# Kernel tuning notes

Hardware: AMD Instinct MI355X
Metric: run time of the kernel (lower is better)

## Reference

```python
import jax, jax.numpy as jnp
import numpy as np

N_EMBD = 768
N_HEAD = 12
EPS = 1e-5


def _layernorm(x, g, b):
    mu = jnp.mean(x, axis=-1, keepdims=True)
    var = jnp.var(x, axis=-1, keepdims=True)
    return (x - mu) * jax.lax.rsqrt(var + EPS) * g + b


def setup_inputs() -> dict:
    key = jax.random.key(0)
    ks = jax.random.split(key, 12)
    C = N_EMBD
    s = 0.02
    return {
        "x": jax.random.normal(ks[0], (1, 4096, C), dtype=jnp.float32),
        "ln1_g": jnp.ones((C,), jnp.float32),
        "ln1_b": jnp.zeros((C,), jnp.float32),
        "w_attn": jax.random.normal(ks[1], (C, 3 * C), jnp.float32) * s,
        "b_attn": jnp.zeros((3 * C,), jnp.float32),
        "w_ao": jax.random.normal(ks[2], (C, C), jnp.float32) * s,
        "b_ao": jnp.zeros((C,), jnp.float32),
        "ln2_g": jnp.ones((C,), jnp.float32),
        "ln2_b": jnp.zeros((C,), jnp.float32),
        "w_fc": jax.random.normal(ks[3], (C, 4 * C), jnp.float32) * s,
        "b_fc": jnp.zeros((4 * C,), jnp.float32),
        "w_proj": jax.random.normal(ks[4], (4 * C, C), jnp.float32) * s,
        "b_proj": jnp.zeros((C,), jnp.float32),
    }


def reference(x, ln1_g, ln1_b, w_attn, b_attn, w_ao, b_ao,
              ln2_g, ln2_b, w_fc, b_fc, w_proj, b_proj):
    B, T, C = x.shape
    H = N_HEAD
    D = C // H

    # ---- attention sub-block ----
    h = _layernorm(x, ln1_g, ln1_b)
    qkv = h @ w_attn + b_attn                      # [B,T,3C]
    q, k, v = jnp.split(qkv, 3, axis=-1)
    q = q.reshape(B, T, H, D).transpose(0, 2, 1, 3)  # [B,H,T,D]
    k = k.reshape(B, T, H, D).transpose(0, 2, 1, 3)
    v = v.reshape(B, T, H, D).transpose(0, 2, 1, 3)
    att = jnp.einsum('bhqd,bhkd->bhqk', q, k) * (1.0 / jnp.sqrt(jnp.float32(D)))
    att = jax.nn.softmax(att, axis=-1)             # no causal mask in source
    y = jnp.einsum('bhqk,bhkd->bhqd', att, v)      # [B,H,T,D]
    y = y.transpose(0, 2, 1, 3).reshape(B, T, C)
    x = x + y @ w_ao + b_ao

    # ---- MLP sub-block ----
    h = _layernorm(x, ln2_g, ln2_b)
    h = jax.nn.gelu(h @ w_fc + b_fc, approximate=False)  # torch F.gelu = exact
    x = x + h @ w_proj + b_proj
    return x
```

## Files before the change

### kernel.cpp

```cpp
#include <hip/hip_runtime.h>
#include <hip/hip_bf16.h>
#include <cstdint>
#include <cstddef>

typedef __hip_bfloat16 bf16;
typedef __attribute__((ext_vector_type(8))) short short8;
typedef __attribute__((ext_vector_type(4))) float f32x4;
typedef __attribute__((ext_vector_type(16))) float f32x16;

#define C_EMBD 768
#define C3     2304
#define T_SEQ  4096
#define NHEAD  12
#define KVSPLIT 2

__device__ __forceinline__ void load16(const void* g, void* lds) {
  __builtin_amdgcn_global_load_lds(
      (const __attribute__((address_space(1))) uint32_t*)g,
      (__attribute__((address_space(3))) uint32_t*)lds, 16, 0, 0);
}

__device__ __forceinline__ short f2bf_bits(float x) {
  union { bf16 h; short s; } u; u.h = __float2bfloat16(x); return u.s;
}

__device__ __forceinline__ float bfbits2f(short s) {
  union { uint32_t u; float f; } u; u.u = ((uint32_t)(unsigned short)s) << 16; return u.f;
}

__device__ __forceinline__ float max3f(float a, float b, float c) {
  float d;
  asm("v_max3_f32 %0, %1, %2, %3" : "=v"(d) : "v"(a), "v"(b), "v"(c));
  return d;
}

#if __has_builtin(__builtin_amdgcn_exp2f)
#define QK_SCALE (0.125f * 1.44269504088896340736f)
__device__ __forceinline__ float expx(float x) { return __builtin_amdgcn_exp2f(x); }
#else
#define QK_SCALE 0.125f
__device__ __forceinline__ float expx(float x) { return __expf(x); }
#endif

__global__ __launch_bounds__(256) void ln_kernel(const float* __restrict__ x,
    const float* __restrict__ g, const float* __restrict__ b, bf16* __restrict__ out) {
  const int row = blockIdx.x;
  const int tid = threadIdx.x;
  const int lane = tid & 63, wave = tid >> 6;
  const float* xr = x + (size_t)row * C_EMBD;
  float v[3];
  #pragma unroll
  for (int i = 0; i < 3; ++i) v[i] = xr[tid + i * 256];
  float s = v[0] + v[1] + v[2];
  #pragma unroll
  for (int o = 1; o < 64; o <<= 1) s += __shfl_xor(s, o, 64);
  __shared__ float red[4];
  if (lane == 0) red[wave] = s;
  __syncthreads();
  const float mu = (red[0] + red[1] + red[2] + red[3]) * (1.0f / C_EMBD);
  float d0 = v[0] - mu, d1 = v[1] - mu, d2 = v[2] - mu;
  float q = d0 * d0 + d1 * d1 + d2 * d2;
  #pragma unroll
  for (int o = 1; o < 64; o <<= 1) q += __shfl_xor(q, o, 64);
  __syncthreads();
  if (lane == 0) red[wave] = q;
  __syncthreads();
  const float var = (red[0] + red[1] + red[2] + red[3]) * (1.0f / C_EMBD);
  const float rs = rsqrtf(var + 1e-5f);
  #pragma unroll
  for (int i = 0; i < 3; ++i) {
    int c = tid + i * 256;
    out[(size_t)row * C_EMBD + c] = __float2bfloat16((v[i] - mu) * rs * g[c] + b[c]);
  }
}

__global__ __launch_bounds__(256) void transpose4_kernel(
    const float* __restrict__ wA, bf16* __restrict__ oA,
    const float* __restrict__ wB, bf16* __restrict__ oB,
    const float* __restrict__ wC, bf16* __restrict__ oC,
    const float* __restrict__ wD, bf16* __restrict__ oD) {
  __shared__ float tile[32][33];
  int b = blockIdx.x;
  const float* in; bf16* out; int R, C;
  if (b < 1728)      { in = wA; out = oA; R = 768;  C = 2304; }
  else if (b < 2304) { b -= 1728; in = wB; out = oB; R = 768;  C = 768;  }
  else if (b < 4608) { b -= 2304; in = wC; out = oC; R = 768;  C = 3072; }
  else               { b -= 4608; in = wD; out = oD; R = 3072; C = 768;  }
  const int ntx = C / 32;
  const int bx = (b % ntx) * 32;
  const int by = (b / ntx) * 32;
  const int tx = threadIdx.x, ty = threadIdx.y;
  #pragma unroll
  for (int i = 0; i < 32; i += 8)
    tile[ty + i][tx] = in[(size_t)(by + ty + i) * C + bx + tx];
  __syncthreads();
  #pragma unroll
  for (int i = 0; i < 32; i += 8)
    out[(size_t)(bx + ty + i) * R + by + tx] = __float2bfloat16(tile[tx][ty + i]);
}

template <int EPI>
__global__ __launch_bounds__(256, 2) void gemm_bt(
    const bf16* __restrict__ A, const bf16* __restrict__ BT,
    const float* __restrict__ bias, const float* __restrict__ res,
    void* __restrict__ outp, float* __restrict__ outp2, int M, int N, int Ks, int Kst) {
  __shared__ __align__(16) short sA[128 * 32];
  __shared__ __align__(16) short sB[128 * 32];
  const int tid = threadIdx.x;
  const int wave = tid >> 6, lane = tid & 63;
  const int qr = lane >> 4, qm = lane & 15;
  const int wr = wave >> 1, wc = wave & 1;
  const int tM = blockIdx.y * 128, tN = blockIdx.x * 128;
  const int z = (EPI == 4) ? blockIdx.z : 0;

  f32x4 acc[4][4] = {};

  const int srow = tid >> 2;
  const int scol = (tid & 3) * 8;
  const bf16* gA = A + (size_t)z * Ks + (size_t)(tM + srow) * Kst + scol;
  const bf16* gB = BT + (size_t)z * Ks + (size_t)(tN + srow) * Kst + scol;
  char* ldsAw = (char*)sA + wave * 1024;
  char* ldsBw = (char*)sB + wave * 1024;
  const size_t rowskip = (size_t)64 * Kst;

  const int nk = Ks >> 5;
  for (int k0 = 0; k0 < nk; ++k0) {
    __syncthreads();
    load16(gA, ldsAw);
    load16(gA + rowskip, ldsAw + 4096);
    load16(gB, ldsBw);
    load16(gB + rowskip, ldsBw + 4096);
    gA += 32; gB += 32;
    __syncthreads();
    short8 a[4], bb[4];
    #pragma unroll
    for (int i = 0; i < 4; ++i) {
      a[i]  = *(const short8*)&sA[(wr * 64 + i * 16 + qm) * 32 + qr * 8];
      bb[i] = *(const short8*)&sB[(wc * 64 + i * 16 + qm) * 32 + qr * 8];
    }
    #pragma unroll
    for (int mi = 0; mi < 4; ++mi)
      #pragma unroll
      for (int ni = 0; ni < 4; ++ni)
        acc[mi][ni] = __builtin_amdgcn_mfma_f32_16x16x32_bf16(a[mi], bb[ni], acc[mi][ni], 0, 0, 0);
  }

  float* outf = (float*)outp;
  bf16* outh = (bf16*)outp;
  float* po = (EPI == 4) ? ((z == 0) ? (float*)outp : outp2) : nullptr;
  #pragma unroll
  for (int mi = 0; mi < 4; ++mi) {
    #pragma unroll
    for (int ni = 0; ni < 4; ++ni) {
      const int col = tN + wc * 64 + ni * 16 + qm;
      const float bv = (EPI == 4) ? 0.f : bias[col];
      #pragma unroll
      for (int r = 0; r < 4; ++r) {
        const int row = tM + wr * 64 + mi * 16 + qr * 4 + r;
        const size_t idx = (size_t)row * N + col;
        float v = acc[mi][ni][r] + bv;
        if constexpr (EPI == 4) {
          po[idx] = v;
        } else if constexpr (EPI == 1) {
          outf[idx] = v + res[idx];
        } else if constexpr (EPI == 2) {
          v = 0.5f * v * (1.0f + erff(v * 0.70710678118654752f));
          outh[idx] = __float2bfloat16(v);
        } else {
          outh[idx] = __float2bfloat16(v);
        }
      }
    }
  }
}

__global__ __launch_bounds__(256) void splitk_combine(const float* p0,
    const float* __restrict__ p1, const float* __restrict__ res,
    const float* __restrict__ bias, float* out) {
  const int row = blockIdx.x;
  const int tid = threadIdx.x;
  #pragma unroll
  for (int i = 0; i < 3; ++i) {
    const int c = tid + i * 256;
    const size_t idx = (size_t)row * C_EMBD + c;
    out[idx] = p0[idx] + p1[idx] + res[idx] + bias[c];
  }
}

__global__ __launch_bounds__(256, 2) void attn_kernel(const bf16* __restrict__ qkv,
                                                      float* __restrict__ pacc,
                                                      float* __restrict__ pml) {
  __shared__ __align__(16) char sKb[2 * 8192];
  __shared__ __align__(16) char sVb[2 * 8192];
  __shared__ float sRed[4 * 32];

  const int tid = threadIdx.x;
  const int wave = tid >> 6, lane = tid & 63;
  const int qi = lane & 31;
  const int hi = lane >> 5;
  const int hi16 = hi * 16;
  const int head = blockIdx.y;
  const int z = blockIdx.z;
  const int qw = blockIdx.x * 128 + wave * 32;

  short8 qf[4];
  {
    const bf16* qrow = qkv + (size_t)(qw + qi) * C3 + head * 64;
    #pragma unroll
    for (int kd = 0; kd < 4; ++kd) {
      short8 v = *(const short8*)(qrow + kd * 16 + hi * 8);
      #pragma unroll
      for (int i = 0; i < 8; ++i) v[i] = f2bf_bits(bfbits2f(v[i]) * QK_SCALE);
      qf[kd] = v;
    }
  }

  f32x16 acc0 = {}, acc1 = {};
  float m = -3.0e38f, l = 0.f;
  short8 pfrag[4];

  const int nt = (T_SEQ / 64) / KVSPLIT;
  const size_t tilestep = (size_t)64 * C3;
  const size_t zoff = (size_t)z * nt * tilestep;
  const int ksrow = tid >> 3;
  const int kswz = ((tid & 7) ^ (ksrow & 7)) * 8;
  const bf16* gk_base = qkv + zoff + (size_t)ksrow * C3 + C_EMBD + head * 64 + kswz;
  const int vp = tid & 31;
  const int vd0 = (tid >> 5) * 8;
  const bf16* gv_base = qkv + zoff + (size_t)(2 * vp) * C3 + 2 * C_EMBD + head * 64 + vd0;

  const int krow0 = qi * 128;
  const int krow_swz = (qi & 7) << 4;
  const int d1 = 32 + qi;
  const int vs0 = ((qi & 7) ^ ((qi >> 3) & 7)) << 4;
  const int vs1 = ((d1 & 7) ^ ((d1 >> 3) & 7)) << 4;

  short8 v0 = *(const short8*)gv_base;
  short8 v1 = *(const short8*)(gv_base + C3);
  load16(gk_base, sKb + wave * 1024);
  load16(gk_base + (size_t)32 * C3, sKb + wave * 1024 + 4096);

  for (int t = 0; t < nt; ++t) {
    const int cur = t & 1;
    char* bK = sKb + cur * 8192;
    char* bV = sVb + cur * 8192;

    __syncthreads();

    #pragma unroll
    for (int j = 0; j < 8; ++j) {
      const int d = vd0 + j;
      const int vs = ((d & 7) ^ ((d >> 3) & 7)) << 4;
      const uint32_t packed = (uint32_t)(unsigned short)v0[j] |
                              ((uint32_t)(unsigned short)v1[j] << 16);
      *(uint32_t*)(bV + d * 128 + ((vp * 4) ^ vs)) = packed;
    }

    if (t + 1 < nt) {
      const bf16* gv = gv_base + (size_t)(t + 1) * tilestep;
      v0 = *(const short8*)gv;
      v1 = *(const short8*)(gv + C3);
      const bf16* gk = gk_base + (size_t)(t + 1) * tilestep;
      char* bKn = sKb + (cur ^ 1) * 8192;
      load16(gk, bKn + wave * 1024);
      load16(gk + (size_t)32 * C3, bKn + wave * 1024 + 4096);
    }

    f32x16 s0 = {}, s1 = {};
    __builtin_amdgcn_s_setprio(1);
    #pragma unroll
    for (int kd = 0; kd < 4; ++kd) {
      const int off = (kd * 32 + hi16) ^ krow_swz;
      short8 ka0 = *(const short8*)(bK + krow0 + off);
      short8 ka1 = *(const short8*)(bK + 4096 + krow0 + off);
      s0 = __builtin_amdgcn_mfma_f32_32x32x16_bf16(ka0, qf[kd], s0, 0, 0, 0);
      s1 = __builtin_amdgcn_mfma_f32_32x32x16_bf16(ka1, qf[kd], s1, 0, 0, 0);
    }

    if (t > 0) {
      char* bVp = sVb + (cur ^ 1) * 8192;
      #pragma unroll
      for (int kk = 0; kk < 4; ++kk) {
        const int voff = (kk * 32 + hi16);
        short8 vb0 = *(const short8*)(bVp + qi * 128 + (voff ^ vs0));
        short8 vb1 = *(const short8*)(bVp + d1 * 128 + (voff ^ vs1));
        acc0 = __builtin_amdgcn_mfma_f32_32x32x16_bf16(pfrag[kk], vb0, acc0, 0, 0, 0);
        acc1 = __builtin_amdgcn_mfma_f32_32x32x16_bf16(pfrag[kk], vb1, acc1, 0, 0, 0);
      }
    }
    __builtin_amdgcn_s_setprio(0);

    float t8[8];
    #pragma unroll
    for (int i = 0; i < 8; ++i) t8[i] = max3f(s0[i], s0[i + 8], s1[i]);
    float t4[4];
    #pragma unroll
    for (int i = 0; i < 4; ++i) t4[i] = max3f(t8[2 * i], t8[2 * i + 1], s1[8 + i]);
    float t2[2];
    #pragma unroll
    for (int i = 0; i < 2; ++i) t2[i] = max3f(t4[2 * i], t4[2 * i + 1], s1[12 + i]);
    const float t1 = max3f(t2[0], t2[1], s1[14]);
    const float tmx = fmaxf(t1, s1[15]);
    float pmax;
    {
      float a0 = tmx, a1 = tmx;
      asm("v_permlane32_swap_b32 %0, %1" : "+v"(a0), "+v"(a1));
      pmax = fmaxf(a0, a1);
    }

    if (__any(pmax - m > 8.0f)) {
      const float mn = fmaxf(m, pmax);
      const float sc = expx(m - mn);
      l *= sc;
      if (lane < 32) sRed[wave * 32 + qi] = sc;
      #pragma unroll
      for (int r = 0; r < 16; ++r) {
        const float sv = sRed[wave * 32 + ((r & 3) + 8 * (r >> 2) + hi * 4)];
        acc0[r] *= sv; acc1[r] *= sv;
      }
      m = mn;
    }

    float red[16];
    #pragma unroll
    for (int r = 0; r < 16; ++r) { s0[r] = expx(s0[r] - m); s1[r] = expx(s1[r] - m); }
    #pragma unroll
    for (int r = 0; r < 16; ++r) red[r] = s0[r] + s1[r];
    #pragma unroll
    for (int w = 8; w >= 1; w >>= 1)
      #pragma unroll
      for (int r = 0; r < w; ++r) red[r] += red[r + w];
    {
      float a0 = red[0], a1 = red[0];
      asm("v_permlane32_swap_b32 %0, %1" : "+v"(a0), "+v"(a1));
      l += a0 + a1;
    }

    #pragma unroll
    for (int b = 0; b < 2; ++b) {
      const f32x16 sb = b ? s1 : s0;
      uint32_t pk[8];
      #pragma unroll
      for (int g = 0; g < 4; ++g) {
        asm("v_cvt_pk_bf16_f32 %0, %1, %2" : "=v"(pk[2 * g])     : "v"(sb[4 * g + 0]), "v"(sb[4 * g + 1]));
        asm("v_cvt_pk_bf16_f32 %0, %1, %2" : "=v"(pk[2 * g + 1]) : "v"(sb[4 * g + 2]), "v"(sb[4 * g + 3]));
      }
      #pragma unroll
      for (int kbl = 0; kbl < 2; ++kbl) {
        uint32_t w0 = pk[4 * kbl + 0], w2 = pk[4 * kbl + 2];
        asm("v_permlane32_swap_b32 %0, %1" : "+v"(w0), "+v"(w2));
        uint32_t w1 = pk[4 * kbl + 1], w3 = pk[4 * kbl + 3];
        asm("v_permlane32_swap_b32 %0, %1" : "+v"(w1), "+v"(w3));
        union { uint32_t u[4]; short8 v; } pu;
        pu.u[0] = w0; pu.u[1] = w1; pu.u[2] = w2; pu.u[3] = w3;
        pfrag[b * 2 + kbl] = pu.v;
      }
    }
  }

  __syncthreads();
  {
    char* bVl = sVb + ((nt - 1) & 1) * 8192;
    __builtin_amdgcn_s_setprio(1);
    #pragma unroll
    for (int kk = 0; kk < 4; ++kk) {
      const int voff = (kk * 32 + hi16);
      short8 vb0 = *(const short8*)(bVl + qi * 128 + (voff ^ vs0));
      short8 vb1 = *(const short8*)(bVl + d1 * 128 + (voff ^ vs1));
      acc0 = __builtin_amdgcn_mfma_f32_32x32x16_bf16(pfrag[kk], vb0, acc0, 0, 0, 0);
      acc1 = __builtin_amdgcn_mfma_f32_32x32x16_bf16(pfrag[kk], vb1, acc1, 0, 0, 0);
    }
    __builtin_amdgcn_s_setprio(0);
  }

  float* pa = pacc + ((size_t)z * T_SEQ + qw) * C_EMBD + head * 64;
  #pragma unroll
  for (int r = 0; r < 16; ++r) {
    const int q = (r & 3) + 8 * (r >> 2) + hi * 4;
    pa[(size_t)q * C_EMBD + qi]      = acc0[r];
    pa[(size_t)q * C_EMBD + 32 + qi] = acc1[r];
  }
  if (lane < 32) {
    float2* mlp = (float2*)pml;
    mlp[((size_t)z * NHEAD + head) * T_SEQ + qw + qi] = make_float2(m, l);
  }
}

__global__ __launch_bounds__(256) void attn_combine(const float* __restrict__ pacc,
    const float* __restrict__ pml, bf16* __restrict__ out) {
  const int q = blockIdx.x;
  const int tid = threadIdx.x;
  const float2* mlp = (const float2*)pml;
  #pragma unroll
  for (int i = 0; i < 3; ++i) {
    const int c = tid + i * 256;
    const int h = c >> 6;
    const float2 ml0 = mlp[(size_t)h * T_SEQ + q];
    const float2 ml1 = mlp[((size_t)NHEAD + h) * T_SEQ + q];
    const float M = fmaxf(ml0.x, ml1.x);
    const float w0 = expx(ml0.x - M), w1 = expx(ml1.x - M);
    const float inv = 1.0f / (ml0.y * w0 + ml1.y * w1);
    const float a0 = pacc[(size_t)q * C_EMBD + c];
    const float a1 = pacc[(size_t)T_SEQ * C_EMBD + (size_t)q * C_EMBD + c];
    out[(size_t)q * C_EMBD + c] = __float2bfloat16((a0 * w0 + a1 * w1) * inv);
  }
}

extern "C" void kernel_launch(void* const* d_in, const int* in_sizes, int n_in,
                              void* d_out, int out_size, void* d_ws, size_t ws_size,
                              hipStream_t stream) {
  const float* x      = (const float*)d_in[0];
  const float* ln1_g  = (const float*)d_in[1];
  const float* ln1_b  = (const float*)d_in[2];
  const float* w_attn = (const float*)d_in[3];
  const float* b_attn = (const float*)d_in[4];
  const float* w_ao   = (const float*)d_in[5];
  const float* b_ao   = (const float*)d_in[6];
  const float* ln2_g  = (const float*)d_in[7];
  const float* ln2_b  = (const float*)d_in[8];
  const float* w_fc   = (const float*)d_in[9];
  const float* b_fc   = (const float*)d_in[10];
  const float* w_proj = (const float*)d_in[11];
  const float* b_proj = (const float*)d_in[12];

  char* ws = (char*)d_ws;
  size_t off = 0;
  auto alloc = [&](size_t nbytes) {
    char* p = ws + off;
    off += (nbytes + 255) & ~(size_t)255;
    return p;
  };
  bf16* wT_attn = (bf16*)alloc((size_t)C3 * C_EMBD * 2);
  bf16* wT_ao   = (bf16*)alloc((size_t)C_EMBD * C_EMBD * 2);
  bf16* wT_fc   = (bf16*)alloc((size_t)4 * C_EMBD * C_EMBD * 2);
  bf16* wT_proj = (bf16*)alloc((size_t)C_EMBD * 4 * C_EMBD * 2);
  bf16* h       = (bf16*)alloc((size_t)T_SEQ * C_EMBD * 2);
  bf16* qkv     = (bf16*)alloc((size_t)T_SEQ * C3 * 2);
  bf16* y       = (bf16*)alloc((size_t)T_SEQ * C_EMBD * 2);
  float* x1     = (float*)alloc((size_t)T_SEQ * C_EMBD * 4);
  bf16* hf      = (bf16*)alloc((size_t)T_SEQ * 4 * C_EMBD * 2);
  float* pml    = (float*)alloc((size_t)KVSPLIT * NHEAD * T_SEQ * 2 * 4);
  float* pacc   = (float*)hf;
  float* pp0    = (float*)d_out;
  float* pp1    = (float*)qkv;
  (void)ws_size; (void)in_sizes; (void)n_in; (void)out_size;

  transpose4_kernel<<<6912, dim3(32, 8), 0, stream>>>(w_attn, wT_attn, w_ao, wT_ao,
                                                      w_fc, wT_fc, w_proj, wT_proj);

  ln_kernel<<<T_SEQ, 256, 0, stream>>>(x, ln1_g, ln1_b, h);
  gemm_bt<0><<<dim3(C3 / 128, T_SEQ / 128), 256, 0, stream>>>(h, wT_attn, b_attn, nullptr, qkv,
                                                              nullptr, T_SEQ, C3, C_EMBD, C_EMBD);
  attn_kernel<<<dim3(T_SEQ / 128, NHEAD, KVSPLIT), 256, 0, stream>>>(qkv, pacc, pml);
  attn_combine<<<T_SEQ, 256, 0, stream>>>(pacc, pml, y);
  gemm_bt<1><<<dim3(C_EMBD / 128, T_SEQ / 128), 256, 0, stream>>>(y, wT_ao, b_ao, x, x1,
                                                                  nullptr, T_SEQ, C_EMBD,
                                                                  C_EMBD, C_EMBD);
  ln_kernel<<<T_SEQ, 256, 0, stream>>>(x1, ln2_g, ln2_b, h);
  gemm_bt<2><<<dim3(4 * C_EMBD / 128, T_SEQ / 128), 256, 0, stream>>>(h, wT_fc, b_fc, nullptr, hf,
                                                                      nullptr, T_SEQ, 4 * C_EMBD,
                                                                      C_EMBD, C_EMBD);
  gemm_bt<4><<<dim3(C_EMBD / 128, T_SEQ / 128, 2), 256, 0, stream>>>(hf, wT_proj, nullptr, nullptr,
                                                                     pp0, pp1, T_SEQ, C_EMBD,
                                                                     2 * C_EMBD, 4 * C_EMBD);
  splitk_combine<<<T_SEQ, 256, 0, stream>>>(pp0, pp1, x1, b_proj, (float*)d_out);
}
```

Before: 235.9 us.

## Double-buffer GEMM LDS tiles and split-K attention output projection fused into LN2

Converts the GEMM main loop to a two-stage LDS double buffer, so the next K-slice's global-to-LDS loads are issued while the current slice's MFMAs run, with one barrier per iteration instead of two. The attention output projection now runs as a split-K GEMM over two halves, giving a grid of twice as many blocks for this small-N GEMM. A new fused kernel sums the two partials, residual and bias, writes x1, and applies the second layernorm, which replaces the separate LN launch. Costs are doubled LDS per block, which could reduce occupancy, plus extra partial-buffer traffic through the reused hf workspace.

```diff
diff --git a/kernel.cpp b/kernel.cpp
--- a/kernel.cpp
+++ b/kernel.cpp
@@ -51,6 +51,45 @@
   float v[3];
   #pragma unroll
   for (int i = 0; i < 3; ++i) v[i] = xr[tid + i * 256];
+  float s = v[0] + v[1] + v[2];
+  #pragma unroll
+  for (int o = 1; o < 64; o <<= 1) s += __shfl_xor(s, o, 64);
+  __shared__ float red[4];
+  if (lane == 0) red[wave] = s;
+  __syncthreads();
+  const float mu = (red[0] + red[1] + red[2] + red[3]) * (1.0f / C_EMBD);
+  float d0 = v[0] - mu, d1 = v[1] - mu, d2 = v[2] - mu;
+  float q = d0 * d0 + d1 * d1 + d2 * d2;
+  #pragma unroll
+  for (int o = 1; o < 64; o <<= 1) q += __shfl_xor(q, o, 64);
+  __syncthreads();
+  if (lane == 0) red[wave] = q;
+  __syncthreads();
+  const float var = (red[0] + red[1] + red[2] + red[3]) * (1.0f / C_EMBD);
+  const float rs = rsqrtf(var + 1e-5f);
+  #pragma unroll
+  for (int i = 0; i < 3; ++i) {
+    int c = tid + i * 256;
+    out[(size_t)row * C_EMBD + c] = __float2bfloat16((v[i] - mu) * rs * g[c] + b[c]);
+  }
+}
+
+__global__ __launch_bounds__(256) void ln2_fused_kernel(
+    const float* __restrict__ pa0, const float* __restrict__ pa1,
+    const float* __restrict__ x, const float* __restrict__ b_ao,
+    const float* __restrict__ g, const float* __restrict__ b,
+    bf16* __restrict__ out, float* __restrict__ x1) {
+  const int row = blockIdx.x;
+  const int tid = threadIdx.x;
+  const int lane = tid & 63, wave = tid >> 6;
+  float v[3];
+  #pragma unroll
+  for (int i = 0; i < 3; ++i) {
+    const int c = tid + i * 256;
+    const size_t idx = (size_t)row * C_EMBD + c;
+    v[i] = pa0[idx] + pa1[idx] + x[idx] + b_ao[c];
+    x1[idx] = v[i];
+  }
   float s = v[0] + v[1] + v[2];
   #pragma unroll
   for (int o = 1; o < 64; o <<= 1) s += __shfl_xor(s, o, 64);
@@ -104,8 +143,8 @@
     const bf16* __restrict__ A, const bf16* __restrict__ BT,
     const float* __restrict__ bias, const float* __restrict__ res,
     void* __restrict__ outp, float* __restrict__ outp2, int M, int N, int Ks, int Kst) {
-  __shared__ __align__(16) short sA[128 * 32];
-  __shared__ __align__(16) short sB[128 * 32];
+  __shared__ __align__(16) short sA[2][128 * 32];
+  __shared__ __align__(16) short sB[2][128 * 32];
   const int tid = threadIdx.x;
   const int wave = tid >> 6, lane = tid & 63;
   const int qr = lane >> 4, qm = lane & 15;
@@ -119,30 +158,47 @@
   const int scol = (tid & 3) * 8;
   const bf16* gA = A + (size_t)z * Ks + (size_t)(tM + srow) * Kst + scol;
   const bf16* gB = BT + (size_t)z * Ks + (size_t)(tN + srow) * Kst + scol;
-  char* ldsAw = (char*)sA + wave * 1024;
-  char* ldsBw = (char*)sB + wave * 1024;
+  const int woff = wave * 1024;
   const size_t rowskip = (size_t)64 * Kst;
 
   const int nk = Ks >> 5;
+  {
+    char* la = (char*)sA[0] + woff;
+    char* lb = (char*)sB[0] + woff;
+    load16(gA, la);
+    load16(gA + rowskip, la + 4096);
+    load16(gB, lb);
+    load16(gB + rowskip, lb + 4096);
+    gA += 32; gB += 32;
+  }
+  __syncthreads();
+
+  int cur = 0;
   for (int k0 = 0; k0 < nk; ++k0) {
-    __syncthreads();
-    load16(gA, ldsAw);
-    load16(gA + rowskip, ldsAw + 4096);
-    load16(gB, ldsBw);
-    load16(gB + rowskip, ldsBw + 4096);
-    gA += 32; gB += 32;
-    __syncthreads();
+    if (k0 + 1 < nk) {
+      char* la = (char*)sA[cur ^ 1] + woff;
+      char* lb = (char*)sB[cur ^ 1] + woff;
+      load16(gA, la);
+      load16(gA + rowskip, la + 4096);
+      load16(gB, lb);
+      load16(gB + rowskip, lb + 4096);
+      gA += 32; gB += 32;
+    }
+    const short* bufA = sA[cur];
+    const short* bufB = sB[cur];
     short8 a[4], bb[4];
     #pragma unroll
     for (int i = 0; i < 4; ++i) {
-      a[i]  = *(const short8*)&sA[(wr * 64 + i * 16 + qm) * 32 + qr * 8];
-      bb[i] = *(const short8*)&sB[(wc * 64 + i * 16 + qm) * 32 + qr * 8];
+      a[i]  = *(const short8*)&bufA[(wr * 64 + i * 16 + qm) * 32 + qr * 8];
+      bb[i] = *(const short8*)&bufB[(wc * 64 + i * 16 + qm) * 32 + qr * 8];
     }
     #pragma unroll
     for (int mi = 0; mi < 4; ++mi)
       #pragma unroll
       for (int ni = 0; ni < 4; ++ni)
         acc[mi][ni] = __builtin_amdgcn_mfma_f32_16x16x32_bf16(a[mi], bb[ni], acc[mi][ni], 0, 0, 0);
+    __syncthreads();
+    cur ^= 1;
   }
 
   float* outf = (float*)outp;
@@ -161,8 +217,6 @@
         float v = acc[mi][ni][r] + bv;
         if constexpr (EPI == 4) {
           po[idx] = v;
-        } else if constexpr (EPI == 1) {
-          outf[idx] = v + res[idx];
         } else if constexpr (EPI == 2) {
           v = 0.5f * v * (1.0f + erff(v * 0.70710678118654752f));
           outh[idx] = __float2bfloat16(v);
@@ -172,6 +226,7 @@
       }
     }
   }
+  (void)outf; (void)res;
 }
 
 __global__ __launch_bounds__(256) void splitk_combine(const float* p0,
@@ -441,6 +496,8 @@
   bf16* hf      = (bf16*)alloc((size_t)T_SEQ * 4 * C_EMBD * 2);
   float* pml    = (float*)alloc((size_t)KVSPLIT * NHEAD * T_SEQ * 2 * 4);
   float* pacc   = (float*)hf;
+  float* pa0    = (float*)hf;
+  float* pa1    = (float*)hf + (size_t)T_SEQ * C_EMBD;
   float* pp0    = (float*)d_out;
   float* pp1    = (float*)qkv;
   (void)ws_size; (void)in_sizes; (void)n_in; (void)out_size;
@@ -453,10 +510,10 @@
                                                               nullptr, T_SEQ, C3, C_EMBD, C_EMBD);
   attn_kernel<<<dim3(T_SEQ / 128, NHEAD, KVSPLIT), 256, 0, stream>>>(qkv, pacc, pml);
   attn_combine<<<T_SEQ, 256, 0, stream>>>(pacc, pml, y);
-  gemm_bt<1><<<dim3(C_EMBD / 128, T_SEQ / 128), 256, 0, stream>>>(y, wT_ao, b_ao, x, x1,
-                                                                  nullptr, T_SEQ, C_EMBD,
-                                                                  C_EMBD, C_EMBD);
-  ln_kernel<<<T_SEQ, 256, 0, stream>>>(x1, ln2_g, ln2_b, h);
+  gemm_bt<4><<<dim3(C_EMBD / 128, T_SEQ / 128, 2), 256, 0, stream>>>(y, wT_ao, nullptr, nullptr,
+                                                                     pa0, pa1, T_SEQ, C_EMBD,
+                                                                     C_EMBD / 2, C_EMBD);
+  ln2_fused_kernel<<<T_SEQ, 256, 0, stream>>>(pa0, pa1, x, b_ao, ln2_g, ln2_b, h, x1);
   gemm_bt<2><<<dim3(4 * C_EMBD / 128, T_SEQ / 128), 256, 0, stream>>>(h, wT_fc, b_fc, nullptr, hf,
                                                                       nullptr, T_SEQ, 4 * C_EMBD,
                                                                       C_EMBD, C_EMBD);
```

Result: faster. 228.3 us (-3.2%).
